# Performance work log

Measured on AMD Instinct MI355X. Metric: run time of the kernel, lower is better.

The kernel has to match this reference:

```python
import jax, jax.numpy as jnp
from jax import lax
import numpy as np

D = 640
HID = 64
DROP_RATIO = 0.1
N_ITER = int(D * DROP_RATIO)  # 64
TEMP = 0.07
EPS = 1e-7


def setup_inputs() -> dict:
    key = jax.random.key(0)
    k_x, k_w1, k_b1, k_w2, k_b2 = jax.random.split(key, 5)
    B = 8192
    x = jax.random.normal(k_x, (B, D), dtype=jnp.float32)
    # torch Linear default init: U(-1/sqrt(fan_in), 1/sqrt(fan_in))
    lim1 = 1.0 / np.sqrt(D)
    lim2 = 1.0 / np.sqrt(HID)
    W1 = jax.random.uniform(k_w1, (D, HID), minval=-lim1, maxval=lim1, dtype=jnp.float32)
    b1 = jax.random.uniform(k_b1, (HID,), minval=-lim1, maxval=lim1, dtype=jnp.float32)
    W2 = jax.random.uniform(k_w2, (HID, D), minval=-lim2, maxval=lim2, dtype=jnp.float32)
    b2 = jax.random.uniform(k_b2, (D,), minval=-lim2, maxval=lim2, dtype=jnp.float32)
    return {"x": x, "W1": W1, "b1": b1, "W2": W2, "b2": b2}


def reference(x, W1, b1, W2, b2):
    # small MLP: 640 -> 64 -> relu -> 640
    h = jnp.maximum(x @ W1 + b1, 0.0) @ W2 + b2  # (B, 640)

    def step(hhat, _):
        m = 1.0 - hhat
        mhat = jnp.log(m + EPS)
        yhat = jax.nn.softmax((-h + mhat) / TEMP, axis=-1)
        return hhat + yhat * m, None

    hhat0 = jnp.zeros_like(h)
    hhat, _ = lax.scan(jax.checkpoint(step), hhat0, None, length=N_ITER)
    mask = 1.0 - hhat
    return mask * x
```

## Files before the change

kernel.cpp:

```cpp
#include <hip/hip_runtime.h>

#define D 640
#define HID 64
#define NITER 64
#define ROWS 4
#define BLOCK 256

__device__ __forceinline__ float wave_sum(float v) {
#pragma unroll
    for (int off = 32; off; off >>= 1) v += __shfl_xor(v, off);
    return v;
}

__device__ __forceinline__ float pow_main(float y) {
    float p = -2255.638f;
    p = fmaf(p, y, 1096.4908f);
    p = fmaf(p, y, -388.62974f);
    p = fmaf(p, y, 94.897959f);
    p = fmaf(p, y, -14.2857143f);
    p = fmaf(p, y, 1.0f);
    return p;
}
__device__ __forceinline__ float pow_frac(float y) {
    float q = -0.0293926f;
    q = fmaf(q, y, -0.0395668f);
    q = fmaf(q, y, -0.0583090f);
    q = fmaf(q, y, -0.1020408f);
    q = fmaf(q, y, -0.2857143f);
    q = fmaf(q, y, 1.0f);
    return q;
}

__global__ __launch_bounds__(BLOCK) void dimmask_kernel(
    const float* __restrict__ x, const float* __restrict__ W1,
    const float* __restrict__ b1, const float* __restrict__ W2,
    const float* __restrict__ b2, float* __restrict__ out)
{
    constexpr float INV_T = 1.0f / 0.07f;
    constexpr float LOG2E = 1.4426950408889634f;
    constexpr float TEMP  = 0.07f;

    __shared__ float lds_a[ROWS][D];
    __shared__ float lds_part[4][ROWS][HID];
    __shared__ float lds_hid[ROWS][HID];

    const int tid  = threadIdx.x;
    const int row0 = blockIdx.x * ROWS;

    {
        const float4* xv  = (const float4*)(x + (size_t)row0 * D);
        float4*       lxv = (float4*)(&lds_a[0][0]);
        for (int i = tid; i < ROWS * D / 4; i += BLOCK) lxv[i] = xv[i];
    }
    __syncthreads();

    {
        const int k = tid & 63, c = tid >> 6;
        float acc[ROWS] = {0.f, 0.f, 0.f, 0.f};
        const int t0 = c * (D / 4);
#pragma unroll 4
        for (int t = t0; t < t0 + D / 4; ++t) {
            float w = W1[t * HID + k];
#pragma unroll
            for (int r = 0; r < ROWS; ++r) acc[r] += lds_a[r][t] * w;
        }
#pragma unroll
        for (int r = 0; r < ROWS; ++r) lds_part[c][r][k] = acc[r];
    }
    __syncthreads();
    {
        const int r = tid >> 6, k = tid & 63;
        float s = lds_part[0][r][k] + lds_part[1][r][k]
                + lds_part[2][r][k] + lds_part[3][r][k] + b1[k];
        lds_hid[r][k] = fmaxf(s, 0.f);
    }
    __syncthreads();

    for (int j = tid; j < D; j += BLOCK) {
        float acc[ROWS] = {0.f, 0.f, 0.f, 0.f};
#pragma unroll 8
        for (int k = 0; k < HID; ++k) {
            float w = W2[k * D + j];
#pragma unroll
            for (int r = 0; r < ROWS; ++r) acc[r] += lds_hid[r][k] * w;
        }
        float bb = b2[j];
#pragma unroll
        for (int r = 0; r < ROWS; ++r)
            lds_a[r][j] = fminf(-(acc[r] + bb) * (LOG2E * INV_T), 120.0f);
    }
    __syncthreads();

    const int r = tid >> 6, l = tid & 63;
    float E[10], w[10];
#pragma unroll
    for (int u = 0; u < 10; ++u) {
        E[u] = __builtin_amdgcn_exp2f(lds_a[r][l + 64 * u]);
        w[u] = 1.0f;
    }

    for (int it = 0; it < NITER; ++it) {
        float e[10], s = 0.f;
#pragma unroll
        for (int u = 0; u < 10; ++u) { e[u] = w[u] * E[u]; s += e[u]; }
        s = wave_sum(s);
        float rs = __builtin_amdgcn_rcpf(s);
#pragma unroll
        for (int u = 0; u < 10; ++u) {
            float y = e[u] * rs;
            if (__any(y > 0.03125f)) {
                float f  = fmaxf(fmaf(-e[u], rs, 1.0f), 0.f);
                float f2 = f * f, f4 = f2 * f2, f8 = f4 * f4;
                float f14 = f8 * f4 * f2;
                w[u] *= f14 * pow_frac(y);
            } else {
                w[u] *= pow_main(y);
            }
        }
    }

    const float* xrow = x + (size_t)(row0 + r) * D;
    float* orow = out + (size_t)(row0 + r) * D;
#pragma unroll
    for (int u = 0; u < 10; ++u) {
        int j = l + 64 * u;
        float m = __builtin_amdgcn_exp2f(TEMP * __builtin_amdgcn_logf(w[u]));
        orow[j] = m * xrow[j];
    }
}

extern "C" void kernel_launch(void* const* d_in, const int* in_sizes, int n_in,
                              void* d_out, int out_size, void* d_ws, size_t ws_size,
                              hipStream_t stream) {
    const float* x  = (const float*)d_in[0];
    const float* W1 = (const float*)d_in[1];
    const float* b1 = (const float*)d_in[2];
    const float* W2 = (const float*)d_in[3];
    const float* b2 = (const float*)d_in[4];
    float* out = (float*)d_out;

    const int B = in_sizes[0] / D;
    dim3 grid(B / ROWS), block(BLOCK);
    hipLaunchKernelGGL(dimmask_kernel, grid, block, 0, stream, x, W1, b1, W2, b2, out);
}
```

Before: 207.8 us.

## Use DPP wave reductions, max-shifted exponent, and branchless pow approximation

Replaces the shfl_xor wave sum with DPP row/broadcast reductions plus a readlane, and subtracts the row max before exponentiation instead of clamping. It also replaces the divergent-check branch between two polynomial approximations of (1-y)^(1/T) with a single branchless path (f^14 times a shortened polynomial). The aim is to cut cross-lane communication latency and remove the __any vote and branch in the 64-iteration inner loop. The trade-off is some accuracy, since the truncated polynomial and f^14 form are applied to all values, including small y.

```diff
diff --git a/kernel.cpp b/kernel.cpp
--- a/kernel.cpp
+++ b/kernel.cpp
@@ -6,29 +6,33 @@
 #define ROWS 4
 #define BLOCK 256
 
-__device__ __forceinline__ float wave_sum(float v) {
-#pragma unroll
-    for (int off = 32; off; off >>= 1) v += __shfl_xor(v, off);
-    return v;
+#define DPP_ADD_STEP(v, ctrl, rmask)                                          \
+    v += __builtin_bit_cast(float, __builtin_amdgcn_update_dpp(               \
+             0, __builtin_bit_cast(int, v), ctrl, rmask, 0xf, true))
+#define DPP_MAX_STEP(v, ctrl, rmask)                                          \
+    v = fmaxf(v, __builtin_bit_cast(float, __builtin_amdgcn_update_dpp(       \
+             __builtin_bit_cast(int, v), __builtin_bit_cast(int, v),          \
+             ctrl, rmask, 0xf, false)))
+
+__device__ __forceinline__ float wave_sum_dpp(float v) {
+    DPP_ADD_STEP(v, 0x111, 0xf);
+    DPP_ADD_STEP(v, 0x112, 0xf);
+    DPP_ADD_STEP(v, 0x114, 0xf);
+    DPP_ADD_STEP(v, 0x118, 0xf);
+    DPP_ADD_STEP(v, 0x142, 0xa);
+    DPP_ADD_STEP(v, 0x143, 0xc);
+    return __builtin_bit_cast(float,
+        __builtin_amdgcn_readlane(__builtin_bit_cast(int, v), 63));
 }
-
-__device__ __forceinline__ float pow_main(float y) {
-    float p = -2255.638f;
-    p = fmaf(p, y, 1096.4908f);
-    p = fmaf(p, y, -388.62974f);
-    p = fmaf(p, y, 94.897959f);
-    p = fmaf(p, y, -14.2857143f);
-    p = fmaf(p, y, 1.0f);
-    return p;
-}
-__device__ __forceinline__ float pow_frac(float y) {
-    float q = -0.0293926f;
-    q = fmaf(q, y, -0.0395668f);
-    q = fmaf(q, y, -0.0583090f);
-    q = fmaf(q, y, -0.1020408f);
-    q = fmaf(q, y, -0.2857143f);
-    q = fmaf(q, y, 1.0f);
-    return q;
+__device__ __forceinline__ float wave_max_dpp(float v) {
+    DPP_MAX_STEP(v, 0x111, 0xf);
+    DPP_MAX_STEP(v, 0x112, 0xf);
+    DPP_MAX_STEP(v, 0x114, 0xf);
+    DPP_MAX_STEP(v, 0x118, 0xf);
+    DPP_MAX_STEP(v, 0x142, 0xa);
+    DPP_MAX_STEP(v, 0x143, 0xc);
+    return __builtin_bit_cast(float,
+        __builtin_amdgcn_readlane(__builtin_bit_cast(int, v), 63));
 }
 
 __global__ __launch_bounds__(BLOCK) void dimmask_kernel(
@@ -87,35 +91,47 @@
         float bb = b2[j];
 #pragma unroll
         for (int r = 0; r < ROWS; ++r)
-            lds_a[r][j] = fminf(-(acc[r] + bb) * (LOG2E * INV_T), 120.0f);
+            lds_a[r][j] = -(acc[r] + bb) * (LOG2E * INV_T);
     }
     __syncthreads();
 
     const int r = tid >> 6, l = tid & 63;
     float E[10], w[10];
+    {
+        float ht[10], hmax = -3.0e38f;
 #pragma unroll
-    for (int u = 0; u < 10; ++u) {
-        E[u] = __builtin_amdgcn_exp2f(lds_a[r][l + 64 * u]);
-        w[u] = 1.0f;
+        for (int u = 0; u < 10; ++u) {
+            ht[u] = lds_a[r][l + 64 * u];
+            hmax = fmaxf(hmax, ht[u]);
+        }
+        hmax = wave_max_dpp(hmax);
+#pragma unroll
+        for (int u = 0; u < 10; ++u) {
+            E[u] = __builtin_amdgcn_exp2f(ht[u] - hmax);
+            w[u] = 1.0f;
+        }
     }
 
     for (int it = 0; it < NITER; ++it) {
-        float e[10], s = 0.f;
+        float e[10];
 #pragma unroll
-        for (int u = 0; u < 10; ++u) { e[u] = w[u] * E[u]; s += e[u]; }
-        s = wave_sum(s);
+        for (int u = 0; u < 10; ++u) e[u] = w[u] * E[u];
+        float t0 = e[0] + e[1], t1 = e[2] + e[3], t2 = e[4] + e[5],
+              t3 = e[6] + e[7], t4 = e[8] + e[9];
+        float s = ((t0 + t1) + (t2 + t3)) + t4;
+        s = wave_sum_dpp(s);
         float rs = __builtin_amdgcn_rcpf(s);
 #pragma unroll
         for (int u = 0; u < 10; ++u) {
-            float y = e[u] * rs;
-            if (__any(y > 0.03125f)) {
-                float f  = fmaxf(fmaf(-e[u], rs, 1.0f), 0.f);
-                float f2 = f * f, f4 = f2 * f2, f8 = f4 * f4;
-                float f14 = f8 * f4 * f2;
-                w[u] *= f14 * pow_frac(y);
-            } else {
-                w[u] *= pow_main(y);
-            }
+            float y  = e[u] * rs;
+            float f  = 1.0f - y;
+            float f2 = f * f, f4 = f2 * f2, f8 = f4 * f4;
+            float f14 = f8 * f4 * f2;
+            float p = fmaf(-0.0395668f, y, -0.0583090f);
+            p = fmaf(p, y, -0.1020408f);
+            p = fmaf(p, y, -0.2857143f);
+            p = fmaf(p, y, 1.0f);
+            w[u] *= f14 * p;
         }
     }
 
```

Measured after the change: 215.5 us. 3.7% more time.
